# Kernel tuning notes

Hardware: AMD Instinct MI355X
Metric: run time of the kernel (lower is better)

The kernel has to match this reference:

```python
import jax, jax.numpy as jnp
import numpy as np

LAMBDA_SINK = 0.05  # temperature
NUM_SINK = 10       # Sinkhorn iterations


def setup_inputs() -> dict:
    key = jax.random.key(0)
    log_alpha = jax.random.normal(key, (8, 2048, 2048), dtype=jnp.float32)
    return {"log_alpha": log_alpha}


def reference(log_alpha):
    # gumbel_sinkhorn(log_alpha, temp=lambda_sink, n_iter=num_sink, slack=False)
    la = log_alpha / LAMBDA_SINK

    def body(la, _):
        # row normalization: subtract logsumexp over columns (dim=2)
        la = la - jax.nn.logsumexp(la, axis=2, keepdims=True)
        # column normalization: subtract logsumexp over rows (dim=1)
        la = la - jax.nn.logsumexp(la, axis=1, keepdims=True)
        return la, None

    la, _ = jax.lax.scan(body, la, None, length=NUM_SINK)
    return jnp.exp(la)  # doubly-stochastic (approx) matrix
```

## Files before the change

### kernel.cpp

```cpp
#include <hip/hip_runtime.h>
#include <math.h>

#define NB 8
#define NN 2048
#define SCALE 20.0f
#define RPW 8
#define CH  (NN / RPW)

__device__ __forceinline__ float wave_max(float x) {
#pragma unroll
    for (int off = 32; off >= 1; off >>= 1)
        x = fmaxf(x, __shfl_xor(x, off, 64));
    return x;
}
__device__ __forceinline__ float wave_sum(float x) {
#pragma unroll
    for (int off = 32; off >= 1; off >>= 1)
        x += __shfl_xor(x, off, 64);
    return x;
}

__global__ __launch_bounds__(256) void fused_iter(const float* __restrict__ A,
                                                  const float* __restrict__ v,
                                                  float* __restrict__ u,
                                                  float* __restrict__ ps) {
    const int wid   = threadIdx.x >> 6;
    const int lane  = threadIdx.x & 63;
    const int wg    = blockIdx.x * 4 + wid;
    const int b     = wg / CH;
    const int chunk = wg % CH;
    const int row0  = chunk * RPW;
    const float4* v4 = (const float4*)(v + (size_t)b * NN);

    float s[32];
#pragma unroll
    for (int i = 0; i < 32; ++i) s[i] = 0.f;

#pragma unroll 1
    for (int r = 0; r < RPW; ++r) {
        const float4* a4 = (const float4*)(A + ((size_t)b * NN + row0 + r) * NN);
        float e[32];
        float m = -INFINITY;
#pragma unroll
        for (int k = 0; k < 8; ++k) {
            float4 a  = a4[lane + (k << 6)];
            float4 vv = v4[lane + (k << 6)];
            e[4 * k + 0] = fmaf(a.x, SCALE, -vv.x);
            e[4 * k + 1] = fmaf(a.y, SCALE, -vv.y);
            e[4 * k + 2] = fmaf(a.z, SCALE, -vv.z);
            e[4 * k + 3] = fmaf(a.w, SCALE, -vv.w);
        }
#pragma unroll
        for (int i = 0; i < 32; ++i) m = fmaxf(m, e[i]);
        m = wave_max(m);
        float ls = 0.f;
#pragma unroll
        for (int i = 0; i < 32; ++i) { e[i] = __expf(e[i] - m); ls += e[i]; }
        float S = wave_sum(ls);
        if (lane == 0) u[b * NN + row0 + r] = m + __logf(S);
        float rS = __builtin_amdgcn_rcpf(S);
#pragma unroll
        for (int i = 0; i < 32; ++i) s[i] = fmaf(e[i], rS, s[i]);
    }

    float4* pbase = (float4*)(ps + (size_t)wg * NN);
#pragma unroll
    for (int k = 0; k < 8; ++k)
        pbase[lane + (k << 6)] =
            make_float4(s[4 * k], s[4 * k + 1], s[4 * k + 2], s[4 * k + 3]);
}

__global__ __launch_bounds__(256) void combine(const float* __restrict__ ps,
                                               float* __restrict__ v) {
    const int colg = threadIdx.x & 63;
    const int grp  = threadIdx.x >> 6;
    const int gcol = blockIdx.x * 64 + colg;
    const int b    = gcol >> 11;
    const int col  = gcol & (NN - 1);
    const float* pb = ps + (size_t)b * CH * NN + col + (size_t)grp * (CH / 4) * NN;

    float s0 = 0.f, s1 = 0.f, s2 = 0.f, s3 = 0.f;
#pragma unroll 4
    for (int i = 0; i < CH / 4; i += 4) {
        s0 += pb[(size_t)(i + 0) * NN];
        s1 += pb[(size_t)(i + 1) * NN];
        s2 += pb[(size_t)(i + 2) * NN];
        s3 += pb[(size_t)(i + 3) * NN];
    }
    __shared__ float sm[4][64];
    sm[grp][colg] = (s0 + s1) + (s2 + s3);
    __syncthreads();
    if (threadIdx.x < 64) {
        float t = (sm[0][colg] + sm[1][colg]) + (sm[2][colg] + sm[3][colg]);
        v[gcol] += __logf(t);
    }
}

__global__ __launch_bounds__(256) void row_lse(const float* __restrict__ A,
                                               const float* __restrict__ v,
                                               float* __restrict__ u) {
    const int wid  = threadIdx.x >> 6;
    const int lane = threadIdx.x & 63;
    const int row  = blockIdx.x * 4 + wid;
    const int b    = row >> 11;
    const float4* a4 = (const float4*)(A + (size_t)row * NN);
    const float4* v4 = (const float4*)(v + (size_t)b * NN);
    float x[32];
#pragma unroll
    for (int k = 0; k < 8; ++k) {
        float4 a  = a4[lane + (k << 6)];
        float4 vv = v4[lane + (k << 6)];
        x[4 * k + 0] = fmaf(a.x, SCALE, -vv.x);
        x[4 * k + 1] = fmaf(a.y, SCALE, -vv.y);
        x[4 * k + 2] = fmaf(a.z, SCALE, -vv.z);
        x[4 * k + 3] = fmaf(a.w, SCALE, -vv.w);
    }
    float m = -INFINITY;
#pragma unroll
    for (int i = 0; i < 32; ++i) m = fmaxf(m, x[i]);
    m = wave_max(m);
    float s = 0.f;
#pragma unroll
    for (int i = 0; i < 32; ++i) s += __expf(x[i] - m);
    s = wave_sum(s);
    if (lane == 0) u[row] = m + __logf(s);
}

__global__ __launch_bounds__(256) void col_lse(const float* __restrict__ A,
                                               const float* __restrict__ u,
                                               float* __restrict__ v) {
    const int b    = blockIdx.x >> 6;
    const int tile = blockIdx.x & 63;
    const int ci   = threadIdx.x & 31;
    const int rg   = threadIdx.x >> 5;
    const int col  = (tile << 5) + ci;
    const float* Ab = A + (size_t)b * NN * NN;
    const float* ub = u + b * NN;
    float m0 = -INFINITY, s0 = 0.f, m1 = -INFINITY, s1 = 0.f;
    for (int r = rg; r < NN; r += 16) {
        float x0 = fmaf(Ab[(size_t)r * NN + col], SCALE, -ub[r]);
        float x1 = fmaf(Ab[(size_t)(r + 8) * NN + col], SCALE, -ub[r + 8]);
        float nm0 = fmaxf(m0, x0);
        s0 = s0 * __expf(m0 - nm0) + __expf(x0 - nm0); m0 = nm0;
        float nm1 = fmaxf(m1, x1);
        s1 = s1 * __expf(m1 - nm1) + __expf(x1 - nm1); m1 = nm1;
    }
    float m = fmaxf(m0, m1);
    float s = s0 * __expf(m0 - m) + s1 * __expf(m1 - m);
    __shared__ float sm[8][33];
    __shared__ float ss[8][33];
    sm[rg][ci] = m; ss[rg][ci] = s;
    __syncthreads();
    if (threadIdx.x < 32) {
        const int c = threadIdx.x;
        float M = sm[0][c], S = ss[0][c];
#pragma unroll
        for (int g = 1; g < 8; ++g) {
            float mg = sm[g][c], sg = ss[g][c];
            float nM = fmaxf(M, mg);
            S = S * __expf(M - nM) + sg * __expf(mg - nM);
            M = nM;
        }
        v[b * NN + (tile << 5) + c] = M + __logf(S);
    }
}

__global__ __launch_bounds__(256) void final_exp(const float* __restrict__ A,
                                                 const float* __restrict__ u,
                                                 const float* __restrict__ v,
                                                 float* __restrict__ out) {
    const int i4    = blockIdx.x * 256 + threadIdx.x;
    const int rglob = i4 >> 9;
    const int c4    = i4 & 511;
    const int b     = rglob >> 11;
    const float uu  = u[rglob];
    float4 a  = ((const float4*)A)[i4];
    float4 vv = ((const float4*)(v + (size_t)b * NN))[c4];
    float4 o;
    o.x = __expf(fmaf(a.x, SCALE, -uu) - vv.x);
    o.y = __expf(fmaf(a.y, SCALE, -uu) - vv.y);
    o.z = __expf(fmaf(a.z, SCALE, -uu) - vv.z);
    o.w = __expf(fmaf(a.w, SCALE, -uu) - vv.w);
    ((float4*)out)[i4] = o;
}

extern "C" void kernel_launch(void* const* d_in, const int* in_sizes, int n_in,
                              void* d_out, int out_size, void* d_ws, size_t ws_size,
                              hipStream_t stream) {
    const float* A = (const float*)d_in[0];
    float* out = (float*)d_out;
    float* u  = (float*)d_ws;
    float* v  = u + NB * NN;
    float* ps = v + NB * NN;

    const size_t need = ((size_t)2 * NB * NN + (size_t)NB * CH * NN) * sizeof(float);

    hipMemsetAsync(v, 0, NB * NN * sizeof(float), stream);

    if (ws_size >= need) {
        for (int it = 0; it < 10; ++it) {
            fused_iter<<<NB * CH / 4, 256, 0, stream>>>(A, v, u, ps);
            combine<<<NB * NN / 64, 256, 0, stream>>>(ps, v);
        }
    } else {
        for (int it = 0; it < 10; ++it) {
            row_lse<<<NB * NN / 4, 256, 0, stream>>>(A, v, u);
            col_lse<<<NB * (NN / 32), 256, 0, stream>>>(A, u, v);
        }
    }
    final_exp<<<NB * NN * NN / 1024, 256, 0, stream>>>(A, u, v, out);
}
```

Baseline: 539.3 us.

## Split each row across a whole block with software-prefetched loads

The fused row/column kernel now gives each 256-thread block 8 rows, with the four waves each covering a quarter of every row. Per-row max and sum are merged through shared memory, and the next row's data is prefetched while the current one is processed. This cuts per-thread registers from 32 accumulators to 8, targets higher occupancy via launch bounds, and launches four times as many blocks. The cost is a block-wide barrier per row. The combine kernel is reorganised for the new partial-sum layout, and the final exp kernel uses nontemporal stores.

Result: slower. 720.5 us (+33.6%).

```diff
diff --git a/kernel.cpp b/kernel.cpp
--- a/kernel.cpp
+++ b/kernel.cpp
@@ -4,8 +4,10 @@
 #define NB 8
 #define NN 2048
 #define SCALE 20.0f
-#define RPW 8
-#define CH  (NN / RPW)
+#define RPB 8
+#define CH  (NN / RPB)
+
+typedef float v4f __attribute__((ext_vector_type(4)));
 
 __device__ __forceinline__ float wave_max(float x) {
 #pragma unroll
@@ -20,78 +22,108 @@
     return x;
 }
 
-__global__ __launch_bounds__(256) void fused_iter(const float* __restrict__ A,
-                                                  const float* __restrict__ v,
-                                                  float* __restrict__ u,
-                                                  float* __restrict__ ps) {
-    const int wid   = threadIdx.x >> 6;
+__global__ __launch_bounds__(256, 6) void fused_iter(const float* __restrict__ A,
+                                                     const float* __restrict__ v,
+                                                     float* __restrict__ u,
+                                                     float* __restrict__ ps) {
+    const int w     = threadIdx.x >> 6;
     const int lane  = threadIdx.x & 63;
-    const int wg    = blockIdx.x * 4 + wid;
-    const int b     = wg / CH;
-    const int chunk = wg % CH;
-    const int row0  = chunk * RPW;
+    const int b     = blockIdx.x >> 8;
+    const int chunk = blockIdx.x & (CH - 1);
+    const int row0  = chunk * RPB;
+    const int idx0  = (w << 7) + lane;
+    const int idx1  = idx0 + 64;
+
     const float4* v4 = (const float4*)(v + (size_t)b * NN);
-
-    float s[32];
-#pragma unroll
-    for (int i = 0; i < 32; ++i) s[i] = 0.f;
-
-#pragma unroll 1
-    for (int r = 0; r < RPW; ++r) {
-        const float4* a4 = (const float4*)(A + ((size_t)b * NN + row0 + r) * NN);
-        float e[32];
-        float m = -INFINITY;
-#pragma unroll
-        for (int k = 0; k < 8; ++k) {
-            float4 a  = a4[lane + (k << 6)];
-            float4 vv = v4[lane + (k << 6)];
-            e[4 * k + 0] = fmaf(a.x, SCALE, -vv.x);
-            e[4 * k + 1] = fmaf(a.y, SCALE, -vv.y);
-            e[4 * k + 2] = fmaf(a.z, SCALE, -vv.z);
-            e[4 * k + 3] = fmaf(a.w, SCALE, -vv.w);
-        }
-#pragma unroll
-        for (int i = 0; i < 32; ++i) m = fmaxf(m, e[i]);
+    const float4 vv0 = v4[idx0];
+    const float4 vv1 = v4[idx1];
+
+    const float4* Ab = (const float4*)(A + ((size_t)b * NN + row0) * NN);
+    const int RS = NN / 4;
+
+    __shared__ float lm[RPB][4];
+    __shared__ float lsum[RPB][4];
+
+    float s[8];
+#pragma unroll
+    for (int i = 0; i < 8; ++i) s[i] = 0.f;
+
+    float4 a0 = Ab[idx0];
+    float4 a1 = Ab[idx1];
+
+#pragma unroll
+    for (int r = 0; r < RPB; ++r) {
+        const int rn = (r + 1 < RPB) ? r + 1 : r;
+        float4 na0 = Ab[rn * RS + idx0];
+        float4 na1 = Ab[rn * RS + idx1];
+
+        float x[8];
+        x[0] = fmaf(a0.x, SCALE, -vv0.x);
+        x[1] = fmaf(a0.y, SCALE, -vv0.y);
+        x[2] = fmaf(a0.z, SCALE, -vv0.z);
+        x[3] = fmaf(a0.w, SCALE, -vv0.w);
+        x[4] = fmaf(a1.x, SCALE, -vv1.x);
+        x[5] = fmaf(a1.y, SCALE, -vv1.y);
+        x[6] = fmaf(a1.z, SCALE, -vv1.z);
+        x[7] = fmaf(a1.w, SCALE, -vv1.w);
+
+        float m = x[0];
+#pragma unroll
+        for (int i = 1; i < 8; ++i) m = fmaxf(m, x[i]);
         m = wave_max(m);
+
+        float e[8];
         float ls = 0.f;
 #pragma unroll
-        for (int i = 0; i < 32; ++i) { e[i] = __expf(e[i] - m); ls += e[i]; }
+        for (int i = 0; i < 8; ++i) { e[i] = __expf(x[i] - m); ls += e[i]; }
         float S = wave_sum(ls);
-        if (lane == 0) u[b * NN + row0 + r] = m + __logf(S);
-        float rS = __builtin_amdgcn_rcpf(S);
-#pragma unroll
-        for (int i = 0; i < 32; ++i) s[i] = fmaf(e[i], rS, s[i]);
-    }
-
-    float4* pbase = (float4*)(ps + (size_t)wg * NN);
-#pragma unroll
-    for (int k = 0; k < 8; ++k)
-        pbase[lane + (k << 6)] =
-            make_float4(s[4 * k], s[4 * k + 1], s[4 * k + 2], s[4 * k + 3]);
+
+        if (lane == 0) { lm[r][w] = m; lsum[r][w] = S; }
+        __syncthreads();
+
+        const float m0 = lm[r][0], m1 = lm[r][1], m2 = lm[r][2], m3 = lm[r][3];
+        const float M = fmaxf(fmaxf(m0, m1), fmaxf(m2, m3));
+        const float T = lsum[r][0] * __expf(m0 - M) + lsum[r][1] * __expf(m1 - M)
+                      + lsum[r][2] * __expf(m2 - M) + lsum[r][3] * __expf(m3 - M);
+        if (threadIdx.x == 0) u[b * NN + row0 + r] = M + __logf(T);
+
+        const float scale = __expf(m - M) * __builtin_amdgcn_rcpf(T);
+#pragma unroll
+        for (int i = 0; i < 8; ++i) s[i] = fmaf(e[i], scale, s[i]);
+
+        a0 = na0; a1 = na1;
+    }
+
+    float4* pb = (float4*)(ps + (size_t)blockIdx.x * NN);
+    pb[idx0] = make_float4(s[0], s[1], s[2], s[3]);
+    pb[idx1] = make_float4(s[4], s[5], s[6], s[7]);
 }
 
 __global__ __launch_bounds__(256) void combine(const float* __restrict__ ps,
                                                float* __restrict__ v) {
-    const int colg = threadIdx.x & 63;
-    const int grp  = threadIdx.x >> 6;
-    const int gcol = blockIdx.x * 64 + colg;
+    const int coll = threadIdx.x & 31;
+    const int grp  = threadIdx.x >> 5;
+    const int gcol = blockIdx.x * 32 + coll;
     const int b    = gcol >> 11;
     const int col  = gcol & (NN - 1);
-    const float* pb = ps + (size_t)b * CH * NN + col + (size_t)grp * (CH / 4) * NN;
+    const float* pb = ps + (size_t)b * CH * NN + col;
 
     float s0 = 0.f, s1 = 0.f, s2 = 0.f, s3 = 0.f;
-#pragma unroll 4
-    for (int i = 0; i < CH / 4; i += 4) {
-        s0 += pb[(size_t)(i + 0) * NN];
-        s1 += pb[(size_t)(i + 1) * NN];
-        s2 += pb[(size_t)(i + 2) * NN];
-        s3 += pb[(size_t)(i + 3) * NN];
-    }
-    __shared__ float sm[4][64];
-    sm[grp][colg] = (s0 + s1) + (s2 + s3);
+#pragma unroll
+    for (int i = 0; i < 32; i += 4) {
+        const int c = (grp << 5) + i;
+        s0 += pb[(size_t)(c + 0) * NN];
+        s1 += pb[(size_t)(c + 1) * NN];
+        s2 += pb[(size_t)(c + 2) * NN];
+        s3 += pb[(size_t)(c + 3) * NN];
+    }
+    __shared__ float sm[8][33];
+    sm[grp][coll] = (s0 + s1) + (s2 + s3);
     __syncthreads();
-    if (threadIdx.x < 64) {
-        float t = (sm[0][colg] + sm[1][colg]) + (sm[2][colg] + sm[3][colg]);
+    if (threadIdx.x < 32) {
+        float t = 0.f;
+#pragma unroll
+        for (int g = 0; g < 8; ++g) t += sm[g][threadIdx.x];
         v[gcol] += __logf(t);
     }
 }
@@ -176,12 +208,12 @@
     const float uu  = u[rglob];
     float4 a  = ((const float4*)A)[i4];
     float4 vv = ((const float4*)(v + (size_t)b * NN))[c4];
-    float4 o;
+    v4f o;
     o.x = __expf(fmaf(a.x, SCALE, -uu) - vv.x);
     o.y = __expf(fmaf(a.y, SCALE, -uu) - vv.y);
     o.z = __expf(fmaf(a.z, SCALE, -uu) - vv.z);
     o.w = __expf(fmaf(a.w, SCALE, -uu) - vv.w);
-    ((float4*)out)[i4] = o;
+    __builtin_nontemporal_store(o, (v4f*)out + i4);
 }
 
 extern "C" void kernel_launch(void* const* d_in, const int* in_sizes, int n_in,
@@ -199,8 +231,8 @@
 
     if (ws_size >= need) {
         for (int it = 0; it < 10; ++it) {
-            fused_iter<<<NB * CH / 4, 256, 0, stream>>>(A, v, u, ps);
-            combine<<<NB * NN / 64, 256, 0, stream>>>(ps, v);
+            fused_iter<<<NB * CH, 256, 0, stream>>>(A, v, u, ps);
+            combine<<<NB * NN / 32, 256, 0, stream>>>(ps, v);
         }
     } else {
         for (int it = 0; it < 10; ++it) {
```

## Halve rows per wave, hoist v loads, add nontemporal stores, widen combine

Applied to the files above, without the earlier changes.

Rows per wave drop from 8 to 4, which doubles the number of waves in the fused row pass, and the row loop is now fully unrolled. The column offsets v are loaded once per wave instead of once per row. Partial-sum writes, partial reads in combine, and the final output all use nontemporal builtins to bypass cache pollution. Combine now uses 32 columns by 8 row groups per block. The cost is that the partial-sum buffer doubles in size, so each iteration writes and reads twice as much partial data.

Result: slower. 742.1 us (+37.6%).

```diff
diff --git a/kernel.cpp b/kernel.cpp
--- a/kernel.cpp
+++ b/kernel.cpp
@@ -4,8 +4,10 @@
 #define NB 8
 #define NN 2048
 #define SCALE 20.0f
-#define RPW 8
+#define RPW 4
 #define CH  (NN / RPW)
+
+typedef float v4f __attribute__((ext_vector_type(4)));
 
 __device__ __forceinline__ float wave_max(float x) {
 #pragma unroll
@@ -20,78 +22,88 @@
     return x;
 }
 
-__global__ __launch_bounds__(256) void fused_iter(const float* __restrict__ A,
-                                                  const float* __restrict__ v,
-                                                  float* __restrict__ u,
-                                                  float* __restrict__ ps) {
-    const int wid   = threadIdx.x >> 6;
+__global__ __launch_bounds__(256, 4) void fused_iter(const float* __restrict__ A,
+                                                     const float* __restrict__ v,
+                                                     float* __restrict__ u,
+                                                     float* __restrict__ ps) {
+    const int w     = threadIdx.x >> 6;
     const int lane  = threadIdx.x & 63;
-    const int wg    = blockIdx.x * 4 + wid;
-    const int b     = wg / CH;
-    const int chunk = wg % CH;
+    const int wg    = blockIdx.x * 4 + w;
+    const int b     = wg >> 9;
+    const int chunk = wg & (CH - 1);
     const int row0  = chunk * RPW;
+
     const float4* v4 = (const float4*)(v + (size_t)b * NN);
+    float vv[32];
+#pragma unroll
+    for (int k = 0; k < 8; ++k) {
+        float4 t = v4[lane + (k << 6)];
+        vv[4 * k + 0] = t.x; vv[4 * k + 1] = t.y;
+        vv[4 * k + 2] = t.z; vv[4 * k + 3] = t.w;
+    }
 
     float s[32];
 #pragma unroll
     for (int i = 0; i < 32; ++i) s[i] = 0.f;
 
-#pragma unroll 1
+#pragma unroll
     for (int r = 0; r < RPW; ++r) {
         const float4* a4 = (const float4*)(A + ((size_t)b * NN + row0 + r) * NN);
-        float e[32];
-        float m = -INFINITY;
+        float x[32];
 #pragma unroll
         for (int k = 0; k < 8; ++k) {
-            float4 a  = a4[lane + (k << 6)];
-            float4 vv = v4[lane + (k << 6)];
-            e[4 * k + 0] = fmaf(a.x, SCALE, -vv.x);
-            e[4 * k + 1] = fmaf(a.y, SCALE, -vv.y);
-            e[4 * k + 2] = fmaf(a.z, SCALE, -vv.z);
-            e[4 * k + 3] = fmaf(a.w, SCALE, -vv.w);
-        }
-#pragma unroll
-        for (int i = 0; i < 32; ++i) m = fmaxf(m, e[i]);
+            float4 t = a4[lane + (k << 6)];
+            x[4 * k + 0] = fmaf(t.x, SCALE, -vv[4 * k + 0]);
+            x[4 * k + 1] = fmaf(t.y, SCALE, -vv[4 * k + 1]);
+            x[4 * k + 2] = fmaf(t.z, SCALE, -vv[4 * k + 2]);
+            x[4 * k + 3] = fmaf(t.w, SCALE, -vv[4 * k + 3]);
+        }
+        float m = x[0];
+#pragma unroll
+        for (int i = 1; i < 32; ++i) m = fmaxf(m, x[i]);
         m = wave_max(m);
         float ls = 0.f;
 #pragma unroll
-        for (int i = 0; i < 32; ++i) { e[i] = __expf(e[i] - m); ls += e[i]; }
+        for (int i = 0; i < 32; ++i) { x[i] = __expf(x[i] - m); ls += x[i]; }
         float S = wave_sum(ls);
         if (lane == 0) u[b * NN + row0 + r] = m + __logf(S);
         float rS = __builtin_amdgcn_rcpf(S);
 #pragma unroll
-        for (int i = 0; i < 32; ++i) s[i] = fmaf(e[i], rS, s[i]);
-    }
-
-    float4* pbase = (float4*)(ps + (size_t)wg * NN);
-#pragma unroll
-    for (int k = 0; k < 8; ++k)
-        pbase[lane + (k << 6)] =
-            make_float4(s[4 * k], s[4 * k + 1], s[4 * k + 2], s[4 * k + 3]);
+        for (int i = 0; i < 32; ++i) s[i] = fmaf(x[i], rS, s[i]);
+    }
+
+    v4f* pb = (v4f*)(ps + (size_t)wg * NN);
+#pragma unroll
+    for (int k = 0; k < 8; ++k) {
+        v4f o = {s[4 * k], s[4 * k + 1], s[4 * k + 2], s[4 * k + 3]};
+        __builtin_nontemporal_store(o, pb + lane + (k << 6));
+    }
 }
 
 __global__ __launch_bounds__(256) void combine(const float* __restrict__ ps,
                                                float* __restrict__ v) {
-    const int colg = threadIdx.x & 63;
-    const int grp  = threadIdx.x >> 6;
-    const int gcol = blockIdx.x * 64 + colg;
+    const int coll = threadIdx.x & 31;
+    const int grp  = threadIdx.x >> 5;
+    const int gcol = blockIdx.x * 32 + coll;
     const int b    = gcol >> 11;
     const int col  = gcol & (NN - 1);
-    const float* pb = ps + (size_t)b * CH * NN + col + (size_t)grp * (CH / 4) * NN;
+    const float* pb = ps + (size_t)b * CH * NN + col + (size_t)grp * (CH / 8) * NN;
 
     float s0 = 0.f, s1 = 0.f, s2 = 0.f, s3 = 0.f;
 #pragma unroll 4
-    for (int i = 0; i < CH / 4; i += 4) {
-        s0 += pb[(size_t)(i + 0) * NN];
-        s1 += pb[(size_t)(i + 1) * NN];
-        s2 += pb[(size_t)(i + 2) * NN];
-        s3 += pb[(size_t)(i + 3) * NN];
-    }
-    __shared__ float sm[4][64];
-    sm[grp][colg] = (s0 + s1) + (s2 + s3);
+    for (int i = 0; i < CH / 8; i += 4) {
+        s0 += __builtin_nontemporal_load(pb + (size_t)(i + 0) * NN);
+        s1 += __builtin_nontemporal_load(pb + (size_t)(i + 1) * NN);
+        s2 += __builtin_nontemporal_load(pb + (size_t)(i + 2) * NN);
+        s3 += __builtin_nontemporal_load(pb + (size_t)(i + 3) * NN);
+    }
+    __shared__ float sm[8][33];
+    sm[grp][coll] = (s0 + s1) + (s2 + s3);
     __syncthreads();
-    if (threadIdx.x < 64) {
-        float t = (sm[0][colg] + sm[1][colg]) + (sm[2][colg] + sm[3][colg]);
+    if (threadIdx.x < 32) {
+        float t = 0.f;
+#pragma unroll
+        for (int g = 0; g < 8; ++g) t += sm[g][threadIdx.x];
         v[gcol] += __logf(t);
     }
 }
@@ -176,12 +188,12 @@
     const float uu  = u[rglob];
     float4 a  = ((const float4*)A)[i4];
     float4 vv = ((const float4*)(v + (size_t)b * NN))[c4];
-    float4 o;
+    v4f o;
     o.x = __expf(fmaf(a.x, SCALE, -uu) - vv.x);
     o.y = __expf(fmaf(a.y, SCALE, -uu) - vv.y);
     o.z = __expf(fmaf(a.z, SCALE, -uu) - vv.z);
     o.w = __expf(fmaf(a.w, SCALE, -uu) - vv.w);
-    ((float4*)out)[i4] = o;
+    __builtin_nontemporal_store(o, (v4f*)out + i4);
 }
 
 extern "C" void kernel_launch(void* const* d_in, const int* in_sizes, int n_in,
@@ -200,7 +212,7 @@
     if (ws_size >= need) {
         for (int it = 0; it < 10; ++it) {
             fused_iter<<<NB * CH / 4, 256, 0, stream>>>(A, v, u, ps);
-            combine<<<NB * NN / 64, 256, 0, stream>>>(ps, v);
+            combine<<<NB * NN / 32, 256, 0, stream>>>(ps, v);
         }
     } else {
         for (int it = 0; it < 10; ++it) {
```
